# Optimization experiments

Hardware: AMD Instinct MI355X
Metric: run time of the kernel (lower is better)

## Reference

```python
import jax, jax.numpy as jnp
import numpy as np

N = 100000      # nodes
E = 3200000     # edges (avg degree 32)
F_IN = 256      # input features
HID = 16        # ARMA hidden width (hard-coded in Net)
C = 16          # num classes
K = 2           # ARMA stacks


def _arma_conv(x, src, dst, init_w, root_w, bias, act):
    """ARMAConv with num_layers=1, shared_weights=True (eval mode, no dropout).
    x: [N, F_in]; init_w/root_w: [K, F_in, F_out]; bias: [K, F_out].
    Returns [N, F_out] (mean over K stacks)."""
    n = x.shape[0]
    # gcn_norm with add_self_loops=False: deg from target (col) index
    deg = jax.ops.segment_sum(jnp.ones_like(src, jnp.float32), dst, num_segments=n)
    dinv = jnp.where(deg > 0, jax.lax.rsqrt(jnp.maximum(deg, 1.0)), 0.0)
    norm = dinv[src] * dinv[dst]                      # [E]
    h = jnp.einsum('nf,kfo->nko', x, init_w)          # [N, K, F_out]
    msg = h[src] * norm[:, None, None]                # [E, K, F_out]
    agg = jax.ops.segment_sum(msg, dst, num_segments=n)  # [N, K, F_out]
    root = jnp.einsum('nf,kfo->nko', x, root_w)       # [N, K, F_out]
    out = act(agg + root + bias[None])                # [N, K, F_out]
    return out.mean(axis=1)                           # [N, F_out]


def setup_inputs() -> dict:
    key = jax.random.key(0)
    ks = jax.random.split(key, 8)
    x = jax.random.normal(ks[0], (N, F_IN), jnp.float32)
    edge_index = jax.random.randint(ks[1], (2, E), 0, N, dtype=jnp.int64)
    s1 = 1.0 / np.sqrt(F_IN)
    s2 = 1.0 / np.sqrt(HID)
    return {
        'x': x,
        'edge_index': edge_index,
        'init_w1': jax.random.normal(ks[2], (K, F_IN, HID), jnp.float32) * s1,
        'root_w1': jax.random.normal(ks[3], (K, F_IN, HID), jnp.float32) * s1,
        'bias1':   jnp.zeros((K, HID), jnp.float32),
        'init_w2': jax.random.normal(ks[4], (K, HID, C), jnp.float32) * s2,
        'root_w2': jax.random.normal(ks[5], (K, HID, C), jnp.float32) * s2,
        'bias2':   jnp.zeros((K, C), jnp.float32),
    }


def reference(x, edge_index, init_w1, root_w1, bias1, init_w2, root_w2, bias2):
    src, dst = edge_index[0], edge_index[1]
    # conv1 uses internal ReLU (ARMAConv default act); Net applies F.relu again
    h = jax.nn.relu(_arma_conv(x, src, dst, init_w1, root_w1, bias1, jax.nn.relu))
    agg_feature = h                                    # detached copy in original
    logits = _arma_conv(h, src, dst, init_w2, root_w2, bias2, lambda t: t)
    return jax.nn.log_softmax(logits, axis=1), agg_feature
```

## Files before the change

### kernel.cpp

```cpp
#include <hip/hip_runtime.h>
#include <cstdint>
#include <cstddef>

#define N_NODES 100000
#define N_EDGES 3200000
#define F_IN    256
#define HID     16
#define KH      32
#define C_OUT   16

#define W_LOG   7
#define W       128
#define NBKT    782
#define CAP     4608
#define EPB     4096

typedef short  bf16x8 __attribute__((ext_vector_type(8)));
typedef float  f32x4  __attribute__((ext_vector_type(4)));
typedef unsigned short u16x8 __attribute__((ext_vector_type(8)));

__device__ __forceinline__ unsigned short f2bf(float f) {
    uint32_t u = __builtin_bit_cast(uint32_t, f);
    u += 0x7fffu + ((u >> 16) & 1u);
    return (unsigned short)(u >> 16);
}
__device__ __forceinline__ float bf2f(unsigned short s) {
    return __builtin_bit_cast(float, (uint32_t)s << 16);
}

__global__ __launch_bounds__(256) void k_part(const int* __restrict__ src,
                                              const int* __restrict__ dst,
                                              int* __restrict__ gcur,
                                              unsigned int* __restrict__ bucketed) {
    __shared__ int hist[NBKT];
    __shared__ int lcur[NBKT];
    __shared__ unsigned int pbuf[EPB];
    __shared__ unsigned short bbuf[EPB];
    int tid = threadIdx.x;
    for (int i = tid; i < NBKT; i += 256) hist[i] = 0;
    __syncthreads();
    int e0 = blockIdx.x * EPB;
    int cnt = min(EPB, N_EDGES - e0);
    for (int i = tid; i < cnt; i += 256) {
        int s = src[e0 + i], d = dst[e0 + i];
        int b = d >> W_LOG;
        pbuf[i] = ((unsigned int)s << W_LOG) | (unsigned int)(d & (W - 1));
        bbuf[i] = (unsigned short)b;
        atomicAdd(&hist[b], 1);
    }
    __syncthreads();
    for (int b = tid; b < NBKT; b += 256) {
        int h = hist[b];
        lcur[b] = h > 0 ? atomicAdd(&gcur[b], h) : 0;
    }
    __syncthreads();
    for (int i = tid; i < cnt; i += 256) {
        int b = bbuf[i];
        int pos = atomicAdd(&lcur[b], 1);
        if (pos < CAP) bucketed[(size_t)b * CAP + pos] = pbuf[i];
    }
}

__global__ __launch_bounds__(256) void k_sort(const unsigned int* __restrict__ bucketed,
                                              const int* __restrict__ gcur,
                                              int* __restrict__ sorted,
                                              int2* __restrict__ meta,
                                              float* __restrict__ dinv) {
    __shared__ int hist[W], pre[W], cur[W];
    __shared__ int sbuf[CAP];
    int tid = threadIdx.x, b = blockIdx.x;
    int cnt = min(gcur[b], CAP);
    const unsigned int* bp = bucketed + (size_t)b * CAP;
    if (tid < W) hist[tid] = 0;
    __syncthreads();
    for (int i = tid; i < cnt; i += 256) atomicAdd(&hist[bp[i] & (W - 1)], 1);
    __syncthreads();
    if (tid < W) pre[tid] = hist[tid];
    __syncthreads();
    for (int off = 1; off < W; off <<= 1) {
        int v = (tid < W && tid >= off) ? pre[tid - off] : 0;
        __syncthreads();
        if (tid < W) pre[tid] += v;
        __syncthreads();
    }
    if (tid < W) cur[tid] = pre[tid] - hist[tid];
    __syncthreads();
    for (int i = tid; i < cnt; i += 256) {
        unsigned int p = bp[i];
        int pos = atomicAdd(&cur[p & (W - 1)], 1);
        sbuf[pos] = (int)(p >> W_LOG);
    }
    __syncthreads();
    int* so = sorted + (size_t)b * CAP;
    for (int i = tid; i < cnt; i += 256) so[i] = sbuf[i];
    int node = b * W + tid;
    if (tid < W && node < N_NODES) {
        int h = hist[tid];
        meta[node] = make_int2(b * CAP + (pre[tid] - h), h);
        dinv[node] = h > 0 ? rsqrtf((float)h) : 0.f;
    }
}

__global__ __launch_bounds__(512) void k_gemm1(
    const float* __restrict__ x, const float* __restrict__ wi,
    const float* __restrict__ wr, const float* __restrict__ dinv,
    unsigned short* __restrict__ h1s0, unsigned short* __restrict__ h1s1,
    float* __restrict__ r1) {
    __shared__ unsigned short wt[64 * 256];
    int tid = threadIdx.x;

    for (int i = tid; i < 8192; i += 512) {
        int ksk = i >> 12, f = (i >> 4) & 255, o = i & 15;
        int col = ksk * 16 + o;
        int slot = (f >> 3) ^ (col & 7);
        wt[col * 256 + slot * 8 + (f & 7)] = f2bf(wi[i]);
    }
    for (int i = tid; i < 8192; i += 512) {
        int ksk = i >> 12, f = (i >> 4) & 255, o = i & 15;
        int col = 32 + ksk * 16 + o;
        int slot = (f >> 3) ^ (col & 7);
        wt[col * 256 + slot * 8 + (f & 7)] = f2bf(wr[i]);
    }
    __syncthreads();

    int lane = tid & 63;
    int wv   = tid >> 6;
    int base = blockIdx.x * 128 + wv * 16;
    int row16 = lane & 15;
    int akg   = lane >> 4;
    int gr = min(base + row16, N_NODES - 1);
    const float* xp = x + (size_t)gr * F_IN + akg * 8;

    f32x4 acc[4] = {{0, 0, 0, 0}, {0, 0, 0, 0}, {0, 0, 0, 0}, {0, 0, 0, 0}};

    #pragma unroll
    for (int ks = 0; ks < 8; ++ks) {
        float4 v0 = *reinterpret_cast<const float4*>(xp + ks * 32);
        float4 v1 = *reinterpret_cast<const float4*>(xp + ks * 32 + 4);
        u16x8 p;
        p[0] = f2bf(v0.x); p[1] = f2bf(v0.y); p[2] = f2bf(v0.z); p[3] = f2bf(v0.w);
        p[4] = f2bf(v1.x); p[5] = f2bf(v1.y); p[6] = f2bf(v1.z); p[7] = f2bf(v1.w);
        bf16x8 af = __builtin_bit_cast(bf16x8, p);
        #pragma unroll
        for (int c = 0; c < 4; ++c) {
            int col = c * 16 + row16;
            int slot = (ks * 4 + akg) ^ (col & 7);
            bf16x8 bfr = *reinterpret_cast<const bf16x8*>(&wt[col * 256 + slot * 8]);
            acc[c] = __builtin_amdgcn_mfma_f32_16x16x32_bf16(af, bfr, acc[c], 0, 0, 0);
        }
    }

    float dv[4];
    #pragma unroll
    for (int r = 0; r < 4; ++r) {
        int n = base + (lane >> 4) * 4 + r;
        dv[r] = (n < N_NODES) ? dinv[n] : 0.f;
    }
    #pragma unroll
    for (int c = 0; c < 4; ++c) {
        #pragma unroll
        for (int r = 0; r < 4; ++r) {
            int n = base + (lane >> 4) * 4 + r;
            if (n < N_NODES) {
                int col = c * 16 + row16;
                float v = acc[c][r];
                if (col < 16)      h1s0[(size_t)n * HID + col] = f2bf(v * dv[r]);
                else if (col < 32) h1s1[(size_t)n * HID + (col - 16)] = f2bf(v * dv[r]);
                else               r1[(size_t)n * KH + (col - 32)] = v;
            }
        }
    }
}

__global__ __launch_bounds__(256) void k_gath(
    const int* __restrict__ sorted, const int2* __restrict__ meta,
    const float* __restrict__ dinv, const unsigned short* __restrict__ tab,
    float* __restrict__ agg) {
    int t = blockIdx.x * 256 + threadIdx.x;
    int n = t >> 2, q = t & 3;
    if (n >= N_NODES) return;
    int2 m = meta[n];
    const int* sp = sorted + m.x;
    float ax = 0, ay = 0, az = 0, aw = 0;
    int j = 0;
    for (; j + 4 <= m.y; j += 4) {
        int s0 = sp[j], s1 = sp[j + 1], s2 = sp[j + 2], s3 = sp[j + 3];
        ushort4 v0 = *reinterpret_cast<const ushort4*>(tab + (size_t)s0 * HID + q * 4);
        ushort4 v1 = *reinterpret_cast<const ushort4*>(tab + (size_t)s1 * HID + q * 4);
        ushort4 v2 = *reinterpret_cast<const ushort4*>(tab + (size_t)s2 * HID + q * 4);
        ushort4 v3 = *reinterpret_cast<const ushort4*>(tab + (size_t)s3 * HID + q * 4);
        ax += (bf2f(v0.x) + bf2f(v1.x)) + (bf2f(v2.x) + bf2f(v3.x));
        ay += (bf2f(v0.y) + bf2f(v1.y)) + (bf2f(v2.y) + bf2f(v3.y));
        az += (bf2f(v0.z) + bf2f(v1.z)) + (bf2f(v2.z) + bf2f(v3.z));
        aw += (bf2f(v0.w) + bf2f(v1.w)) + (bf2f(v2.w) + bf2f(v3.w));
    }
    for (; j < m.y; ++j) {
        int s0 = sp[j];
        ushort4 v0 = *reinterpret_cast<const ushort4*>(tab + (size_t)s0 * HID + q * 4);
        ax += bf2f(v0.x); ay += bf2f(v0.y); az += bf2f(v0.z); aw += bf2f(v0.w);
    }
    float dn = dinv[n];
    *reinterpret_cast<float4*>(agg + (size_t)n * HID + q * 4) =
        make_float4(ax * dn, ay * dn, az * dn, aw * dn);
}

__global__ void k_post1(const float* __restrict__ agg1a, const float* __restrict__ agg1b,
                        const float* __restrict__ r1, const float* __restrict__ b1,
                        const float* __restrict__ wi2, const float* __restrict__ wr2,
                        const float* __restrict__ dinv,
                        float* __restrict__ hout, unsigned short* __restrict__ h2t,
                        float* __restrict__ r2m) {
    int n = blockIdx.x * blockDim.x + threadIdx.x;
    if (n >= N_NODES) return;
    const float4* aa = reinterpret_cast<const float4*>(agg1a + (size_t)n * HID);
    const float4* ab = reinterpret_cast<const float4*>(agg1b + (size_t)n * HID);
    const float4* r4 = reinterpret_cast<const float4*>(r1 + (size_t)n * KH);
    float z[KH];
    #pragma unroll
    for (int qq = 0; qq < 4; ++qq) {
        float4 a0 = aa[qq], a1 = ab[qq], g0 = r4[qq], g1 = r4[4 + qq];
        z[qq * 4 + 0] = a0.x + g0.x;  z[qq * 4 + 1] = a0.y + g0.y;
        z[qq * 4 + 2] = a0.z + g0.z;  z[qq * 4 + 3] = a0.w + g0.w;
        z[16 + qq * 4 + 0] = a1.x + g1.x;  z[16 + qq * 4 + 1] = a1.y + g1.y;
        z[16 + qq * 4 + 2] = a1.z + g1.z;  z[16 + qq * 4 + 3] = a1.w + g1.w;
    }
    float h[HID];
    #pragma unroll
    for (int o = 0; o < HID; ++o) {
        float z0 = fmaxf(z[o] + b1[o], 0.f);
        float z1 = fmaxf(z[16 + o] + b1[16 + o], 0.f);
        h[o] = 0.5f * (z0 + z1);
    }
    float4* ho4 = reinterpret_cast<float4*>(hout + (size_t)n * HID);
    #pragma unroll
    for (int qq = 0; qq < 4; ++qq)
        ho4[qq] = make_float4(h[qq * 4], h[qq * 4 + 1], h[qq * 4 + 2], h[qq * 4 + 3]);
    float dn = dinv[n];
    #pragma unroll
    for (int o = 0; o < HID; ++o) {
        float ai = 0.f, ar = 0.f;
        #pragma unroll
        for (int i = 0; i < HID; ++i) {
            float wim = 0.5f * (wi2[i * 16 + o] + wi2[256 + i * 16 + o]);
            float wrm = 0.5f * (wr2[i * 16 + o] + wr2[256 + i * 16 + o]);
            ai += h[i] * wim;
            ar += h[i] * wrm;
        }
        h2t[(size_t)n * HID + o] = f2bf(ai * dn);
        r2m[(size_t)n * HID + o] = ar;
    }
}

__global__ void k_post2(const float* __restrict__ agg2, const float* __restrict__ r2m,
                        const float* __restrict__ b2, float* __restrict__ out) {
    int n = blockIdx.x * blockDim.x + threadIdx.x;
    if (n >= N_NODES) return;
    const float4* aa = reinterpret_cast<const float4*>(agg2 + (size_t)n * HID);
    const float4* g4 = reinterpret_cast<const float4*>(r2m + (size_t)n * HID);
    float z[C_OUT];
    float mx = -1e30f;
    #pragma unroll
    for (int qq = 0; qq < 4; ++qq) {
        float4 a = aa[qq], g = g4[qq];
        z[qq * 4 + 0] = a.x + g.x;  z[qq * 4 + 1] = a.y + g.y;
        z[qq * 4 + 2] = a.z + g.z;  z[qq * 4 + 3] = a.w + g.w;
    }
    #pragma unroll
    for (int o = 0; o < C_OUT; ++o) {
        z[o] += 0.5f * (b2[o] + b2[16 + o]);
        mx = fmaxf(mx, z[o]);
    }
    float s = 0.f;
    #pragma unroll
    for (int o = 0; o < C_OUT; ++o) s += expf(z[o] - mx);
    float ls = logf(s);
    float4* o4 = reinterpret_cast<float4*>(out + (size_t)n * C_OUT);
    #pragma unroll
    for (int qq = 0; qq < 4; ++qq)
        o4[qq] = make_float4(z[qq * 4] - mx - ls, z[qq * 4 + 1] - mx - ls,
                             z[qq * 4 + 2] - mx - ls, z[qq * 4 + 3] - mx - ls);
}

extern "C" void kernel_launch(void* const* d_in, const int* in_sizes, int n_in,
                              void* d_out, int out_size, void* d_ws, size_t ws_size,
                              hipStream_t stream) {
    const float* x   = (const float*)d_in[0];
    const int*   ei  = (const int*)d_in[1];
    const float* wi1 = (const float*)d_in[2];
    const float* wr1 = (const float*)d_in[3];
    const float* b1  = (const float*)d_in[4];
    const float* wi2 = (const float*)d_in[5];
    const float* wr2 = (const float*)d_in[6];
    const float* b2  = (const float*)d_in[7];
    float* out = (float*)d_out;

    int* gcur = (int*)d_ws;
    unsigned int* bucketed = (unsigned int*)(gcur + 1024);
    int* sorted = (int*)(bucketed + (size_t)NBKT * CAP);
    int2* meta  = (int2*)(sorted + (size_t)NBKT * CAP);
    float* dinv = (float*)(meta + N_NODES);
    float* r1   = dinv + N_NODES;
    float* r2m  = r1 + (size_t)N_NODES * KH;
    float* agg1a = r2m + (size_t)N_NODES * HID;
    float* agg1b = agg1a + (size_t)N_NODES * HID;
    unsigned short* h1s0 = (unsigned short*)(agg1b + (size_t)N_NODES * HID);
    unsigned short* h1s1 = h1s0 + (size_t)N_NODES * HID;
    float* agg2 = agg1a;
    unsigned short* h2t = h1s0;

    const int* srcI = ei;
    const int* dstI = ei + N_EDGES;

    hipMemsetAsync(gcur, 0, 1024 * sizeof(int), stream);

    k_part<<<(N_EDGES + EPB - 1) / EPB, 256, 0, stream>>>(srcI, dstI, gcur, bucketed);
    k_sort<<<NBKT, 256, 0, stream>>>(bucketed, gcur, sorted, meta, dinv);
    k_gemm1<<<(N_NODES + 127) / 128, 512, 0, stream>>>(x, wi1, wr1, dinv, h1s0, h1s1, r1);
    int gathGrid = (N_NODES * 4 + 255) / 256;
    k_gath<<<gathGrid, 256, 0, stream>>>(sorted, meta, dinv, h1s0, agg1a);
    k_gath<<<gathGrid, 256, 0, stream>>>(sorted, meta, dinv, h1s1, agg1b);
    k_post1<<<(N_NODES + 255) / 256, 256, 0, stream>>>(agg1a, agg1b, r1, b1, wi2, wr2,
                                                       dinv, out + (size_t)N_NODES * C_OUT,
                                                       h2t, r2m);
    k_gath<<<gathGrid, 256, 0, stream>>>(sorted, meta, dinv, h2t, agg2);
    k_post2<<<(N_NODES + 255) / 256, 256, 0, stream>>>(agg2, r2m, b2, out);
}
```

Before: 383.2 us.

## Fuse gathers with post-processing and interleave both ARMA stacks in one table

The two per-stack bf16 tables become one interleaved 32-wide table, so a single gather pass with 8 lanes per node covers both stacks. The layer-1 epilogue (bias, ReLU, stack mean, second-layer weight projection) is folded into that gather using cross-lane shuffles and weights staged in shared memory. The layer-2 gather absorbs log-softmax the same way. This drops the float agg intermediates and two kernel launches, and each edge's index list is now read once for layer 1 instead of twice. The cost is more shuffle work and register pressure inside the gather kernels.

```diff
diff --git a/kernel.cpp b/kernel.cpp
--- a/kernel.cpp
+++ b/kernel.cpp
@@ -104,8 +104,7 @@
 __global__ __launch_bounds__(512) void k_gemm1(
     const float* __restrict__ x, const float* __restrict__ wi,
     const float* __restrict__ wr, const float* __restrict__ dinv,
-    unsigned short* __restrict__ h1s0, unsigned short* __restrict__ h1s1,
-    float* __restrict__ r1) {
+    unsigned short* __restrict__ h1c, float* __restrict__ r1) {
     __shared__ unsigned short wt[64 * 256];
     int tid = threadIdx.x;
 
@@ -164,18 +163,98 @@
             if (n < N_NODES) {
                 int col = c * 16 + row16;
                 float v = acc[c][r];
-                if (col < 16)      h1s0[(size_t)n * HID + col] = f2bf(v * dv[r]);
-                else if (col < 32) h1s1[(size_t)n * HID + (col - 16)] = f2bf(v * dv[r]);
-                else               r1[(size_t)n * KH + (col - 32)] = v;
+                if (col < KH) h1c[(size_t)n * KH + col] = f2bf(v * dv[r]);
+                else          r1[(size_t)n * KH + (col - KH)] = v;
             }
         }
     }
 }
 
-__global__ __launch_bounds__(256) void k_gath(
+__global__ __launch_bounds__(512) void k_gath1p(
     const int* __restrict__ sorted, const int2* __restrict__ meta,
-    const float* __restrict__ dinv, const unsigned short* __restrict__ tab,
-    float* __restrict__ agg) {
+    const float* __restrict__ dinv, const unsigned short* __restrict__ h1c,
+    const float* __restrict__ r1, const float* __restrict__ b1,
+    const float* __restrict__ wi2, const float* __restrict__ wr2,
+    float* __restrict__ hout, unsigned short* __restrict__ h2t,
+    float* __restrict__ r2m) {
+    __shared__ float wm[512];
+    int tid = threadIdx.x;
+    if (tid < 256)      wm[tid] = 0.5f * (wi2[tid] + wi2[256 + tid]);
+    else                wm[tid] = 0.5f * (wr2[tid - 256] + wr2[256 + tid - 256]);
+    __syncthreads();
+
+    int t = blockIdx.x * 512 + tid;
+    int n = t >> 3, q = t & 7;
+    if (n >= N_NODES) return;
+    int2 m = meta[n];
+    const int* sp = sorted + m.x;
+    float ax = 0, ay = 0, az = 0, aw = 0;
+    int j = 0;
+    for (; j + 4 <= m.y; j += 4) {
+        int s0 = sp[j], s1 = sp[j + 1], s2 = sp[j + 2], s3 = sp[j + 3];
+        ushort4 v0 = *reinterpret_cast<const ushort4*>(h1c + (size_t)s0 * KH + q * 4);
+        ushort4 v1 = *reinterpret_cast<const ushort4*>(h1c + (size_t)s1 * KH + q * 4);
+        ushort4 v2 = *reinterpret_cast<const ushort4*>(h1c + (size_t)s2 * KH + q * 4);
+        ushort4 v3 = *reinterpret_cast<const ushort4*>(h1c + (size_t)s3 * KH + q * 4);
+        ax += (bf2f(v0.x) + bf2f(v1.x)) + (bf2f(v2.x) + bf2f(v3.x));
+        ay += (bf2f(v0.y) + bf2f(v1.y)) + (bf2f(v2.y) + bf2f(v3.y));
+        az += (bf2f(v0.z) + bf2f(v1.z)) + (bf2f(v2.z) + bf2f(v3.z));
+        aw += (bf2f(v0.w) + bf2f(v1.w)) + (bf2f(v2.w) + bf2f(v3.w));
+    }
+    for (; j < m.y; ++j) {
+        int s0 = sp[j];
+        ushort4 v0 = *reinterpret_cast<const ushort4*>(h1c + (size_t)s0 * KH + q * 4);
+        ax += bf2f(v0.x); ay += bf2f(v0.y); az += bf2f(v0.z); aw += bf2f(v0.w);
+    }
+    float dn = dinv[n];
+    float4 rv = *reinterpret_cast<const float4*>(r1 + (size_t)n * KH + q * 4);
+    float zi[4];
+    zi[0] = fmaxf(ax * dn + rv.x + b1[q * 4 + 0], 0.f);
+    zi[1] = fmaxf(ay * dn + rv.y + b1[q * 4 + 1], 0.f);
+    zi[2] = fmaxf(az * dn + rv.z + b1[q * 4 + 2], 0.f);
+    zi[3] = fmaxf(aw * dn + rv.w + b1[q * 4 + 3], 0.f);
+    float h4[4];
+    #pragma unroll
+    for (int i = 0; i < 4; ++i)
+        h4[i] = 0.5f * (zi[i] + __shfl_xor(zi[i], 4));
+    if (q < 4)
+        *reinterpret_cast<float4*>(hout + (size_t)n * HID + q * 4) =
+            make_float4(h4[0], h4[1], h4[2], h4[3]);
+    int lane = tid & 63;
+    int bl = lane & 56;
+    float hf[16];
+    #pragma unroll
+    for (int jj = 0; jj < 4; ++jj)
+        #pragma unroll
+        for (int i = 0; i < 4; ++i)
+            hf[jj * 4 + i] = __shfl(h4[i], bl + jj);
+    const float* wsel = (q < 4) ? wm : wm + 256;
+    int ocb = (q & 3) * 4;
+    float o4[4] = {0, 0, 0, 0};
+    #pragma unroll
+    for (int k = 0; k < HID; ++k) {
+        float hv = hf[k];
+        o4[0] += hv * wsel[k * 16 + ocb + 0];
+        o4[1] += hv * wsel[k * 16 + ocb + 1];
+        o4[2] += hv * wsel[k * 16 + ocb + 2];
+        o4[3] += hv * wsel[k * 16 + ocb + 3];
+    }
+    if (q < 4) {
+        ushort4 hw;
+        hw.x = f2bf(o4[0] * dn); hw.y = f2bf(o4[1] * dn);
+        hw.z = f2bf(o4[2] * dn); hw.w = f2bf(o4[3] * dn);
+        *reinterpret_cast<ushort4*>(h2t + (size_t)n * HID + ocb) = hw;
+    } else {
+        *reinterpret_cast<float4*>(r2m + (size_t)n * HID + ocb) =
+            make_float4(o4[0], o4[1], o4[2], o4[3]);
+    }
+}
+
+__global__ __launch_bounds__(256) void k_gath2p(
+    const int* __restrict__ sorted, const int2* __restrict__ meta,
+    const float* __restrict__ dinv, const unsigned short* __restrict__ h2t,
+    const float* __restrict__ r2m, const float* __restrict__ b2,
+    float* __restrict__ out) {
     int t = blockIdx.x * 256 + threadIdx.x;
     int n = t >> 2, q = t & 3;
     if (n >= N_NODES) return;
@@ -185,10 +264,10 @@
     int j = 0;
     for (; j + 4 <= m.y; j += 4) {
         int s0 = sp[j], s1 = sp[j + 1], s2 = sp[j + 2], s3 = sp[j + 3];
-        ushort4 v0 = *reinterpret_cast<const ushort4*>(tab + (size_t)s0 * HID + q * 4);
-        ushort4 v1 = *reinterpret_cast<const ushort4*>(tab + (size_t)s1 * HID + q * 4);
-        ushort4 v2 = *reinterpret_cast<const ushort4*>(tab + (size_t)s2 * HID + q * 4);
-        ushort4 v3 = *reinterpret_cast<const ushort4*>(tab + (size_t)s3 * HID + q * 4);
+        ushort4 v0 = *reinterpret_cast<const ushort4*>(h2t + (size_t)s0 * HID + q * 4);
+        ushort4 v1 = *reinterpret_cast<const ushort4*>(h2t + (size_t)s1 * HID + q * 4);
+        ushort4 v2 = *reinterpret_cast<const ushort4*>(h2t + (size_t)s2 * HID + q * 4);
+        ushort4 v3 = *reinterpret_cast<const ushort4*>(h2t + (size_t)s3 * HID + q * 4);
         ax += (bf2f(v0.x) + bf2f(v1.x)) + (bf2f(v2.x) + bf2f(v3.x));
         ay += (bf2f(v0.y) + bf2f(v1.y)) + (bf2f(v2.y) + bf2f(v3.y));
         az += (bf2f(v0.z) + bf2f(v1.z)) + (bf2f(v2.z) + bf2f(v3.z));
@@ -196,89 +275,25 @@
     }
     for (; j < m.y; ++j) {
         int s0 = sp[j];
-        ushort4 v0 = *reinterpret_cast<const ushort4*>(tab + (size_t)s0 * HID + q * 4);
+        ushort4 v0 = *reinterpret_cast<const ushort4*>(h2t + (size_t)s0 * HID + q * 4);
         ax += bf2f(v0.x); ay += bf2f(v0.y); az += bf2f(v0.z); aw += bf2f(v0.w);
     }
     float dn = dinv[n];
-    *reinterpret_cast<float4*>(agg + (size_t)n * HID + q * 4) =
-        make_float4(ax * dn, ay * dn, az * dn, aw * dn);
-}
-
-__global__ void k_post1(const float* __restrict__ agg1a, const float* __restrict__ agg1b,
-                        const float* __restrict__ r1, const float* __restrict__ b1,
-                        const float* __restrict__ wi2, const float* __restrict__ wr2,
-                        const float* __restrict__ dinv,
-                        float* __restrict__ hout, unsigned short* __restrict__ h2t,
-                        float* __restrict__ r2m) {
-    int n = blockIdx.x * blockDim.x + threadIdx.x;
-    if (n >= N_NODES) return;
-    const float4* aa = reinterpret_cast<const float4*>(agg1a + (size_t)n * HID);
-    const float4* ab = reinterpret_cast<const float4*>(agg1b + (size_t)n * HID);
-    const float4* r4 = reinterpret_cast<const float4*>(r1 + (size_t)n * KH);
-    float z[KH];
-    #pragma unroll
-    for (int qq = 0; qq < 4; ++qq) {
-        float4 a0 = aa[qq], a1 = ab[qq], g0 = r4[qq], g1 = r4[4 + qq];
-        z[qq * 4 + 0] = a0.x + g0.x;  z[qq * 4 + 1] = a0.y + g0.y;
-        z[qq * 4 + 2] = a0.z + g0.z;  z[qq * 4 + 3] = a0.w + g0.w;
-        z[16 + qq * 4 + 0] = a1.x + g1.x;  z[16 + qq * 4 + 1] = a1.y + g1.y;
-        z[16 + qq * 4 + 2] = a1.z + g1.z;  z[16 + qq * 4 + 3] = a1.w + g1.w;
-    }
-    float h[HID];
-    #pragma unroll
-    for (int o = 0; o < HID; ++o) {
-        float z0 = fmaxf(z[o] + b1[o], 0.f);
-        float z1 = fmaxf(z[16 + o] + b1[16 + o], 0.f);
-        h[o] = 0.5f * (z0 + z1);
-    }
-    float4* ho4 = reinterpret_cast<float4*>(hout + (size_t)n * HID);
-    #pragma unroll
-    for (int qq = 0; qq < 4; ++qq)
-        ho4[qq] = make_float4(h[qq * 4], h[qq * 4 + 1], h[qq * 4 + 2], h[qq * 4 + 3]);
-    float dn = dinv[n];
-    #pragma unroll
-    for (int o = 0; o < HID; ++o) {
-        float ai = 0.f, ar = 0.f;
-        #pragma unroll
-        for (int i = 0; i < HID; ++i) {
-            float wim = 0.5f * (wi2[i * 16 + o] + wi2[256 + i * 16 + o]);
-            float wrm = 0.5f * (wr2[i * 16 + o] + wr2[256 + i * 16 + o]);
-            ai += h[i] * wim;
-            ar += h[i] * wrm;
-        }
-        h2t[(size_t)n * HID + o] = f2bf(ai * dn);
-        r2m[(size_t)n * HID + o] = ar;
-    }
-}
-
-__global__ void k_post2(const float* __restrict__ agg2, const float* __restrict__ r2m,
-                        const float* __restrict__ b2, float* __restrict__ out) {
-    int n = blockIdx.x * blockDim.x + threadIdx.x;
-    if (n >= N_NODES) return;
-    const float4* aa = reinterpret_cast<const float4*>(agg2 + (size_t)n * HID);
-    const float4* g4 = reinterpret_cast<const float4*>(r2m + (size_t)n * HID);
-    float z[C_OUT];
-    float mx = -1e30f;
-    #pragma unroll
-    for (int qq = 0; qq < 4; ++qq) {
-        float4 a = aa[qq], g = g4[qq];
-        z[qq * 4 + 0] = a.x + g.x;  z[qq * 4 + 1] = a.y + g.y;
-        z[qq * 4 + 2] = a.z + g.z;  z[qq * 4 + 3] = a.w + g.w;
-    }
-    #pragma unroll
-    for (int o = 0; o < C_OUT; ++o) {
-        z[o] += 0.5f * (b2[o] + b2[16 + o]);
-        mx = fmaxf(mx, z[o]);
-    }
-    float s = 0.f;
-    #pragma unroll
-    for (int o = 0; o < C_OUT; ++o) s += expf(z[o] - mx);
+    float4 rv = *reinterpret_cast<const float4*>(r2m + (size_t)n * HID + q * 4);
+    float z[4];
+    z[0] = ax * dn + rv.x + 0.5f * (b2[q * 4 + 0] + b2[16 + q * 4 + 0]);
+    z[1] = ay * dn + rv.y + 0.5f * (b2[q * 4 + 1] + b2[16 + q * 4 + 1]);
+    z[2] = az * dn + rv.z + 0.5f * (b2[q * 4 + 2] + b2[16 + q * 4 + 2]);
+    z[3] = aw * dn + rv.w + 0.5f * (b2[q * 4 + 3] + b2[16 + q * 4 + 3]);
+    float lm = fmaxf(fmaxf(z[0], z[1]), fmaxf(z[2], z[3]));
+    lm = fmaxf(lm, __shfl_xor(lm, 1));
+    float mx = fmaxf(lm, __shfl_xor(lm, 2));
+    float sl = expf(z[0] - mx) + expf(z[1] - mx) + expf(z[2] - mx) + expf(z[3] - mx);
+    sl += __shfl_xor(sl, 1);
+    float s = sl + __shfl_xor(sl, 2);
     float ls = logf(s);
-    float4* o4 = reinterpret_cast<float4*>(out + (size_t)n * C_OUT);
-    #pragma unroll
-    for (int qq = 0; qq < 4; ++qq)
-        o4[qq] = make_float4(z[qq * 4] - mx - ls, z[qq * 4 + 1] - mx - ls,
-                             z[qq * 4 + 2] - mx - ls, z[qq * 4 + 3] - mx - ls);
+    *reinterpret_cast<float4*>(out + (size_t)n * C_OUT + q * 4) =
+        make_float4(z[0] - mx - ls, z[1] - mx - ls, z[2] - mx - ls, z[3] - mx - ls);
 }
 
 extern "C" void kernel_launch(void* const* d_in, const int* in_sizes, int n_in,
@@ -301,12 +316,8 @@
     float* dinv = (float*)(meta + N_NODES);
     float* r1   = dinv + N_NODES;
     float* r2m  = r1 + (size_t)N_NODES * KH;
-    float* agg1a = r2m + (size_t)N_NODES * HID;
-    float* agg1b = agg1a + (size_t)N_NODES * HID;
-    unsigned short* h1s0 = (unsigned short*)(agg1b + (size_t)N_NODES * HID);
-    unsigned short* h1s1 = h1s0 + (size_t)N_NODES * HID;
-    float* agg2 = agg1a;
-    unsigned short* h2t = h1s0;
+    unsigned short* h1c = (unsigned short*)(r2m + (size_t)N_NODES * HID);
+    unsigned short* h2t = h1c + (size_t)N_NODES * KH;
 
     const int* srcI = ei;
     const int* dstI = ei + N_EDGES;
@@ -315,13 +326,10 @@
 
     k_part<<<(N_EDGES + EPB - 1) / EPB, 256, 0, stream>>>(srcI, dstI, gcur, bucketed);
     k_sort<<<NBKT, 256, 0, stream>>>(bucketed, gcur, sorted, meta, dinv);
-    k_gemm1<<<(N_NODES + 127) / 128, 512, 0, stream>>>(x, wi1, wr1, dinv, h1s0, h1s1, r1);
-    int gathGrid = (N_NODES * 4 + 255) / 256;
-    k_gath<<<gathGrid, 256, 0, stream>>>(sorted, meta, dinv, h1s0, agg1a);
-    k_gath<<<gathGrid, 256, 0, stream>>>(sorted, meta, dinv, h1s1, agg1b);
-    k_post1<<<(N_NODES + 255) / 256, 256, 0, stream>>>(agg1a, agg1b, r1, b1, wi2, wr2,
-                                                       dinv, out + (size_t)N_NODES * C_OUT,
-                                                       h2t, r2m);
-    k_gath<<<gathGrid, 256, 0, stream>>>(sorted, meta, dinv, h2t, agg2);
-    k_post2<<<(N_NODES + 255) / 256, 256, 0, stream>>>(agg2, r2m, b2, out);
-}
+    k_gemm1<<<(N_NODES + 127) / 128, 512, 0, stream>>>(x, wi1, wr1, dinv, h1c, r1);
+    k_gath1p<<<(N_NODES * 8 + 511) / 512, 512, 0, stream>>>(
+        sorted, meta, dinv, h1c, r1, b1, wi2, wr2,
+        out + (size_t)N_NODES * C_OUT, h2t, r2m);
+    k_gath2p<<<(N_NODES * 4 + 255) / 256, 256, 0, stream>>>(
+        sorted, meta, dinv, h2t, r2m, b2, out);
+}
```

Result: faster. 331.7 us (-13.4%).
